# Optimization experiments

Measured on AMD Instinct MI355X. Metric: run time of the kernel, lower is better.

The kernel has to match this reference:

```python
import jax, jax.numpy as jnp
import numpy as np

N = 50000
E = 800000
IN_C = 512
HID = 256
NUM_CLASS = (10, 25, 16, 350)


def _glorot(key, shape):
    fan_in, fan_out = shape[0], shape[1]
    lim = float(np.sqrt(6.0 / (fan_in + fan_out)))
    return jax.random.uniform(key, shape, jnp.float32, -lim, lim)


def setup_inputs() -> dict:
    key = jax.random.key(0)
    ks = jax.random.split(key, 16)
    x = jax.random.normal(ks[0], (N, IN_C), jnp.float32)
    edge_index = jax.random.randint(ks[1], (2, E), 0, N, jnp.int32)
    inp = {"x": x, "edge_index": edge_index}
    # gc1
    inp["W1"] = _glorot(ks[2], (IN_C, HID)); inp["b1"] = jnp.zeros((HID,), jnp.float32)
    # four GCNConv heads
    names = ["type", "school", "time", "author"]
    for i, (nm, nc) in enumerate(zip(names, NUM_CLASS)):
        inp[f"Wg_{nm}"] = _glorot(ks[3 + i], (HID, nc))
        inp[f"bg_{nm}"] = jnp.zeros((nc,), jnp.float32)
        inp[f"Wc_{nm}"] = _glorot(ks[7 + i], (nc, nc))
        inp[f"bc_{nm}"] = jnp.zeros((nc,), jnp.float32)
    return inp


def gcn_conv(x, W, b, src, dst, n):
    # GCNConv: out = D^{-1/2} (A + I) D^{-1/2} (x W) + b, symmetric norm.
    xw = x @ W  # [N, out]
    ones = jnp.ones((src.shape[0],), xw.dtype)
    deg = jax.ops.segment_sum(ones, dst, num_segments=n) + 1.0  # +1 from self-loop
    dinv = jax.lax.rsqrt(deg)
    norm = dinv[src] * dinv[dst]  # [E]
    agg = jax.ops.segment_sum(xw[src] * norm[:, None], dst, num_segments=n)
    # self-loop contribution: norm_ii = dinv_i^2
    return agg + xw * (dinv * dinv)[:, None] + b


def reference(x, edge_index, W1, b1,
              Wg_type, bg_type, Wc_type, bc_type,
              Wg_school, bg_school, Wc_school, bc_school,
              Wg_time, bg_time, Wc_time, bc_time,
              Wg_author, bg_author, Wc_author, bc_author):
    src, dst = edge_index[0], edge_index[1]
    n = x.shape[0]
    h = jax.nn.relu(gcn_conv(x, W1, b1, src, dst, n))  # dropout is identity in eval

    def head(Wg, bg, Wc, bc):
        g = gcn_conv(h, Wg, bg, src, dst, n)
        return jax.nn.softmax(g @ Wc + bc, axis=-1)

    out_type = head(Wg_type, bg_type, Wc_type, bc_type)
    out_school = head(Wg_school, bg_school, Wc_school, bc_school)
    out_time = head(Wg_time, bg_time, Wc_time, bc_time)
    out_author = head(Wg_author, bg_author, Wc_author, bc_author)
    return (out_type, out_school, out_time, out_author)
```

## Files before the change

kernel.cpp:

```cpp
#include <hip/hip_runtime.h>
#include <hip/hip_bf16.h>
#include <cstdint>
#include <cstddef>
#include <math.h>

#define NN 50000
#define NE 800000
#define INC 512
#define HIDC 256
#define NBLK ((NN + 255) / 256)

typedef __attribute__((ext_vector_type(8))) short s8v;
typedef __attribute__((ext_vector_type(4))) float f4v;

__device__ __forceinline__ float b2f(unsigned short u) {
    return __uint_as_float(((unsigned)u) << 16);
}
__device__ __forceinline__ unsigned short f2b(float f) {
    __hip_bfloat16 h = __float2bfloat16(f);
    return *reinterpret_cast<unsigned short*>(&h);
}

__global__ void k_deg_count(const int* __restrict__ dst, int* __restrict__ cnt, int e) {
    int i = blockIdx.x * 256 + threadIdx.x;
    if (i < e) atomicAdd(&cnt[dst[i]], 1);
}
__global__ void k_scan1(const int* __restrict__ cnt, int* __restrict__ excl,
                        int* __restrict__ bsum, float* __restrict__ dinv, int n) {
    __shared__ int s[256];
    int i = blockIdx.x * 256 + threadIdx.x;
    int v = (i < n) ? cnt[i] : 0;
    if (i < n) dinv[i] = rsqrtf((float)v + 1.0f);
    s[threadIdx.x] = v;
    __syncthreads();
    for (int off = 1; off < 256; off <<= 1) {
        int t = (threadIdx.x >= off) ? s[threadIdx.x - off] : 0;
        __syncthreads();
        s[threadIdx.x] += t;
        __syncthreads();
    }
    if (i < n) excl[i] = s[threadIdx.x] - v;
    if (threadIdx.x == 255) bsum[blockIdx.x] = s[255];
}
__global__ void k_scan2(int* __restrict__ bsum, int* __restrict__ bsumx, int nb) {
    __shared__ int s[256];
    int t = threadIdx.x;
    int v = (t < nb) ? bsum[t] : 0;
    s[t] = v;
    __syncthreads();
    for (int off = 1; off < 256; off <<= 1) {
        int tt = (t >= off) ? s[t - off] : 0;
        __syncthreads();
        s[t] += tt;
        __syncthreads();
    }
    if (t < nb) bsumx[t] = s[t] - v;
}
__global__ void k_scan3(int* __restrict__ rowptr, const int* __restrict__ bsumx, int n, int e) {
    int i = blockIdx.x * 256 + threadIdx.x;
    if (i < n) rowptr[i] += bsumx[blockIdx.x];
    if (i == 0) rowptr[n] = e;
}
__global__ void k_fill(const int* __restrict__ src, const int* __restrict__ dst,
                       const int* __restrict__ rowptr, int* __restrict__ cursor,
                       int* __restrict__ col, int e) {
    int i = blockIdx.x * 256 + threadIdx.x;
    if (i >= e) return;
    int d = dst[i];
    int pos = rowptr[d] + atomicAdd(&cursor[d], 1);
    col[pos] = src[i];
}

__global__ void k_prep(const float* __restrict__ W1,
                       const float* __restrict__ Wg0, const float* __restrict__ Wc0,
                       const float* __restrict__ bg0, const float* __restrict__ bc0,
                       const float* __restrict__ Wg1, const float* __restrict__ Wc1,
                       const float* __restrict__ bg1, const float* __restrict__ bc1,
                       const float* __restrict__ Wg2, const float* __restrict__ Wc2,
                       const float* __restrict__ bg2, const float* __restrict__ bc2,
                       const float* __restrict__ Wg3, const float* __restrict__ Wc3,
                       const float* __restrict__ bg3, const float* __restrict__ bc3,
                       unsigned short* __restrict__ W1t, unsigned short* __restrict__ Wft,
                       float* __restrict__ bfv)
{
    int b = blockIdx.x, tid = threadIdx.x;
    if (b < 512) {
        int t = b * 256 + tid;
        int c = t >> 9, k = t & 511;
        W1t[t] = f2b(W1[(size_t)k * 256 + c]);
    } else if (b < 960) {
        int j = b - 512, k = tid;
        float s = 0.f;
        if (j < 350)                  { for (int i = 0; i < 350; ++i) s += Wg3[k * 350 + i] * Wc3[(size_t)i * 350 + j]; }
        else if (j >= 352 && j < 362) { int jj = j - 352; for (int i = 0; i < 10; ++i) s += Wg0[k * 10 + i] * Wc0[i * 10 + jj]; }
        else if (j >= 362 && j < 387) { int jj = j - 362; for (int i = 0; i < 25; ++i) s += Wg1[k * 25 + i] * Wc1[i * 25 + jj]; }
        else if (j >= 387 && j < 403) { int jj = j - 387; for (int i = 0; i < 16; ++i) s += Wg2[k * 16 + i] * Wc2[i * 16 + jj]; }
        Wft[j * 256 + k] = f2b(s);
    } else {
        int j = (b - 960) * 256 + tid;
        if (j >= 448) return;
        float s = 0.f;
        if (j < 350)                  { s = bc3[j]; for (int i = 0; i < 350; ++i) s += bg3[i] * Wc3[(size_t)i * 350 + j]; }
        else if (j >= 352 && j < 362) { int jj = j - 352; s = bc0[jj]; for (int i = 0; i < 10; ++i) s += bg0[i] * Wc0[i * 10 + jj]; }
        else if (j >= 362 && j < 387) { int jj = j - 362; s = bc1[jj]; for (int i = 0; i < 25; ++i) s += bg1[i] * Wc1[i * 25 + jj]; }
        else if (j >= 387 && j < 403) { int jj = j - 387; s = bc2[jj]; for (int i = 0; i < 16; ++i) s += bg2[i] * Wc2[i * 16 + jj]; }
        bfv[j] = s;
    }
}

__global__ __launch_bounds__(256) void gemm1_conv(
    const float* __restrict__ X, const unsigned short* __restrict__ Bt,
    unsigned short* __restrict__ C, int M)
{
    __shared__ s8v As[64 * 5];
    __shared__ s8v Bs[256 * 5];
    const int t = threadIdx.x;
    const int lane = t & 63, wv = t >> 6;
    const int row0 = blockIdx.x * 64;
    const int l15 = lane & 15, lq = lane >> 4;

    const int arow = t >> 2, ach = t & 3;
    int gr = row0 + arow; if (gr >= M) gr = M - 1;
    const float* asrc = X + (size_t)gr * 512 + ach * 8;

    f4v acc[16] = {};
    for (int k0 = 0; k0 < 512; k0 += 32) {
        {
            float4 a = *(const float4*)(asrc + k0);
            float4 b = *(const float4*)(asrc + k0 + 4);
            s8v o;
            o[0] = (short)f2b(a.x); o[1] = (short)f2b(a.y);
            o[2] = (short)f2b(a.z); o[3] = (short)f2b(a.w);
            o[4] = (short)f2b(b.x); o[5] = (short)f2b(b.y);
            o[6] = (short)f2b(b.z); o[7] = (short)f2b(b.w);
            As[arow * 5 + ach] = o;
        }
#pragma unroll
        for (int s = 0; s < 4; ++s) {
            int c = s * 256 + t;
            int colr = c >> 2, ch = c & 3;
            Bs[colr * 5 + ch] = *(const s8v*)(Bt + (size_t)colr * 512 + k0 + ch * 8);
        }
        __syncthreads();
        s8v af = As[(wv * 16 + l15) * 5 + lq];
#pragma unroll
        for (int cf = 0; cf < 16; ++cf) {
            s8v bfr = Bs[(cf * 16 + l15) * 5 + lq];
            acc[cf] = __builtin_amdgcn_mfma_f32_16x16x32_bf16(af, bfr, acc[cf], 0, 0, 0);
        }
        __syncthreads();
    }
#pragma unroll
    for (int cf = 0; cf < 16; ++cf)
#pragma unroll
        for (int r = 0; r < 4; ++r) {
            int row = row0 + wv * 16 + lq * 4 + r;
            if (row < M) C[(size_t)row * 256 + cf * 16 + l15] = f2b(acc[cf][r]);
        }
}

template <bool RELU, bool BIAS>
__global__ __launch_bounds__(256) void k_gather2(
    const unsigned short* __restrict__ feat, const int* __restrict__ rowptr,
    const int* __restrict__ col, const float* __restrict__ dinv,
    const float* __restrict__ bias, unsigned short* __restrict__ out, int n)
{
    int unit = (blockIdx.x * 256 + threadIdx.x) >> 5;
    int l32 = threadIdx.x & 31;
    if (unit >= n) return;
    float di = dinv[unit];
    int p0 = rowptr[unit], p1 = rowptr[unit + 1];
    int deg = p1 - p0;
    int myc = 0; float mydj = 0.f;
    if (l32 < deg) { myc = col[p0 + l32]; mydj = dinv[myc]; }
    float acc[8] = {};
    int dmin = deg < 32 ? deg : 32;
    int base = threadIdx.x & 32;
#pragma unroll 2
    for (int q = 0; q < dmin; ++q) {
        int j = __shfl(myc, base + q);
        float dj = __shfl(mydj, base + q);
        s8v v = *(const s8v*)(feat + (size_t)j * HIDC + l32 * 8);
#pragma unroll
        for (int c = 0; c < 8; ++c) acc[c] += dj * b2f((unsigned short)v[c]);
    }
    for (int p = p0 + 32; p < p1; ++p) {
        int j = col[p];
        float dj = dinv[j];
        s8v v = *(const s8v*)(feat + (size_t)j * HIDC + l32 * 8);
#pragma unroll
        for (int c = 0; c < 8; ++c) acc[c] += dj * b2f((unsigned short)v[c]);
    }
    s8v sv = *(const s8v*)(feat + (size_t)unit * HIDC + l32 * 8);
    float dd = di * di;
    s8v o;
#pragma unroll
    for (int c = 0; c < 8; ++c) {
        float r = di * acc[c] + dd * b2f((unsigned short)sv[c]);
        if (BIAS) r += bias[l32 * 8 + c];
        if (RELU) r = fmaxf(r, 0.f);
        o[c] = (short)f2b(r);
    }
    *(s8v*)(out + (size_t)unit * HIDC + l32 * 8) = o;
}

__global__ __launch_bounds__(256) void gemm2_heads(
    const unsigned short* __restrict__ A, const unsigned short* __restrict__ Bt,
    const float* __restrict__ bfv,
    float* __restrict__ o0, float* __restrict__ o1,
    float* __restrict__ o2, float* __restrict__ o3, int M)
{
    __shared__ s8v As[64 * 5];
    __shared__ s8v Bs[448 * 5];
    const int t = threadIdx.x;
    const int lane = t & 63, wv = t >> 6;
    const int row0 = blockIdx.x * 64;
    const int l15 = lane & 15, lq = lane >> 4;

    const int arow = t >> 2, ach = t & 3;
    int gr = row0 + arow; if (gr >= M) gr = M - 1;
    const unsigned short* asrc = A + (size_t)gr * 256 + ach * 8;

    f4v acc[28] = {};
    for (int k0 = 0; k0 < 256; k0 += 32) {
        As[arow * 5 + ach] = *(const s8v*)(asrc + k0);
#pragma unroll
        for (int s = 0; s < 7; ++s) {
            int c = s * 256 + t;
            int colr = c >> 2, ch = c & 3;
            Bs[colr * 5 + ch] = *(const s8v*)(Bt + (size_t)colr * 256 + k0 + ch * 8);
        }
        __syncthreads();
        s8v af = As[(wv * 16 + l15) * 5 + lq];
#pragma unroll
        for (int cf = 0; cf < 28; ++cf) {
            s8v bfr = Bs[(cf * 16 + l15) * 5 + lq];
            acc[cf] = __builtin_amdgcn_mfma_f32_16x16x32_bf16(af, bfr, acc[cf], 0, 0, 0);
        }
        __syncthreads();
    }
#pragma unroll
    for (int cf = 0; cf < 28; ++cf) {
        float b = bfv[cf * 16 + l15];
#pragma unroll
        for (int r = 0; r < 4; ++r) acc[cf][r] += b;
    }
#pragma unroll
    for (int r = 0; r < 4; ++r) {
        int row = row0 + wv * 16 + lq * 4 + r;
        float m0 = -1e30f, m1 = -1e30f, m2 = -1e30f, m3 = -1e30f;
#pragma unroll
        for (int cf = 0; cf < 28; ++cf) {
            int colc = cf * 16 + l15;
            float xv = acc[cf][r];
            if (colc < 350) m0 = fmaxf(m0, xv);
            else if (colc >= 352 && colc < 362) m1 = fmaxf(m1, xv);
            else if (colc >= 362 && colc < 387) m2 = fmaxf(m2, xv);
            else if (colc >= 387 && colc < 403) m3 = fmaxf(m3, xv);
        }
#pragma unroll
        for (int o = 8; o; o >>= 1) {
            m0 = fmaxf(m0, __shfl_xor(m0, o));
            m1 = fmaxf(m1, __shfl_xor(m1, o));
            m2 = fmaxf(m2, __shfl_xor(m2, o));
            m3 = fmaxf(m3, __shfl_xor(m3, o));
        }
        float s0 = 0.f, s1 = 0.f, s2 = 0.f, s3 = 0.f;
#pragma unroll
        for (int cf = 0; cf < 28; ++cf) {
            int colc = cf * 16 + l15;
            float xv = acc[cf][r];
            float e = 0.f;
            if (colc < 350)                     { e = __expf(xv - m0); s0 += e; }
            else if (colc >= 352 && colc < 362) { e = __expf(xv - m1); s1 += e; }
            else if (colc >= 362 && colc < 387) { e = __expf(xv - m2); s2 += e; }
            else if (colc >= 387 && colc < 403) { e = __expf(xv - m3); s3 += e; }
            acc[cf][r] = e;
        }
#pragma unroll
        for (int o = 8; o; o >>= 1) {
            s0 += __shfl_xor(s0, o); s1 += __shfl_xor(s1, o);
            s2 += __shfl_xor(s2, o); s3 += __shfl_xor(s3, o);
        }
        float i0 = 1.f / s0, i1 = 1.f / s1, i2 = 1.f / s2, i3 = 1.f / s3;
        if (row < M) {
#pragma unroll
            for (int cf = 0; cf < 28; ++cf) {
                int colc = cf * 16 + l15;
                float e = acc[cf][r];
                if (colc < 350)                     o3[(size_t)row * 350 + colc]       = e * i0;
                else if (colc >= 352 && colc < 362) o0[(size_t)row * 10 + colc - 352]  = e * i1;
                else if (colc >= 362 && colc < 387) o1[(size_t)row * 25 + colc - 362]  = e * i2;
                else if (colc >= 387 && colc < 403) o2[(size_t)row * 16 + colc - 387]  = e * i3;
            }
        }
    }
}

extern "C" void kernel_launch(void* const* d_in, const int* in_sizes, int n_in,
                              void* d_out, int out_size, void* d_ws, size_t ws_size,
                              hipStream_t stream)
{
    const float* x   = (const float*)d_in[0];
    const int*   ei  = (const int*)d_in[1];
    const float* W1  = (const float*)d_in[2];
    const float* b1  = (const float*)d_in[3];
    const float* Wg0 = (const float*)d_in[4];
    const float* bg0 = (const float*)d_in[5];
    const float* Wc0 = (const float*)d_in[6];
    const float* bc0 = (const float*)d_in[7];
    const float* Wg1 = (const float*)d_in[8];
    const float* bg1 = (const float*)d_in[9];
    const float* Wc1 = (const float*)d_in[10];
    const float* bc1 = (const float*)d_in[11];
    const float* Wg2 = (const float*)d_in[12];
    const float* bg2 = (const float*)d_in[13];
    const float* Wc2 = (const float*)d_in[14];
    const float* bc2 = (const float*)d_in[15];
    const float* Wg3 = (const float*)d_in[16];
    const float* bg3 = (const float*)d_in[17];
    const float* Wc3 = (const float*)d_in[18];
    const float* bc3 = (const float*)d_in[19];
    const int* srcI = ei;
    const int* dstI = ei + NE;

    char* ws = (char*)d_ws;
    size_t off = 0;
    auto alloc = [&](size_t bytes) { void* p = ws + off; off += (bytes + 255) & ~(size_t)255; return p; };
    float* dinv   = (float*)alloc(50176 * 4);
    int*   rowptr = (int*)  alloc(50432 * 4);
    int*   cnt    = (int*)  alloc(2 * 50176 * 4);
    int*   cursor = cnt + 50176;
    int*   bsum   = (int*)  alloc(1024);
    int*   bsumx  = (int*)  alloc(1024);
    int*   col    = (int*)  alloc((size_t)NE * 4);
    unsigned short* W1t = (unsigned short*)alloc(256 * 512 * 2);
    unsigned short* Wft = (unsigned short*)alloc(448 * 256 * 2);
    float* bfv   = (float*)alloc(448 * 4);
    unsigned short* xwb = (unsigned short*)alloc((size_t)NN * HIDC * 2);
    unsigned short* hb  = (unsigned short*)alloc((size_t)NN * HIDC * 2);
    unsigned short* ahb = xwb;

    float* out0 = (float*)d_out;
    float* out1 = out0 + (size_t)NN * 10;
    float* out2 = out1 + (size_t)NN * 25;
    float* out3 = out2 + (size_t)NN * 16;

    hipMemsetAsync(cnt, 0, 2 * 50176 * 4, stream);
    k_deg_count<<<(NE + 255) / 256, 256, 0, stream>>>(dstI, cnt, NE);
    k_scan1<<<NBLK, 256, 0, stream>>>(cnt, rowptr, bsum, dinv, NN);
    k_scan2<<<1, 256, 0, stream>>>(bsum, bsumx, NBLK);
    k_scan3<<<NBLK, 256, 0, stream>>>(rowptr, bsumx, NN, NE);
    k_fill<<<(NE + 255) / 256, 256, 0, stream>>>(srcI, dstI, rowptr, cursor, col, NE);

    k_prep<<<962, 256, 0, stream>>>(W1,
                                    Wg0, Wc0, bg0, bc0, Wg1, Wc1, bg1, bc1,
                                    Wg2, Wc2, bg2, bc2, Wg3, Wc3, bg3, bc3,
                                    W1t, Wft, bfv);

    gemm1_conv<<<(NN + 63) / 64, 256, 0, stream>>>(x, W1t, xwb, NN);
    k_gather2<true, true><<<(NN + 7) / 8, 256, 0, stream>>>(xwb, rowptr, col, dinv, b1, hb, NN);
    k_gather2<false, false><<<(NN + 7) / 8, 256, 0, stream>>>(hb, rowptr, col, dinv, nullptr, ahb, NN);
    gemm2_heads<<<(NN + 63) / 64, 256, 0, stream>>>(ahb, Wft, bfv, out0, out1, out2, out3, NN);
}
```

Before: 328.0 us.

## Swizzle LDS layouts, use direct global-to-LDS loads, retile both GEMMs across waves

Pre-swizzles the bf16 weight matrices (and the aggregated features feeding the head GEMM) into an XOR-swizzled chunk layout, so tiles can be copied straight into LDS with global_load_lds and read without bank conflicts. Both GEMMs now use a 2D wave tiling with 64-wide K steps: two row fragments share each B fragment, which halves LDS fragment reads and cuts the number of barriers. The head GEMM moves to 512 threads and reduces the softmax across waves through shared memory. Weight prep adds a transpose kernel so the 350x350 head-weight fold reads memory coalesced. The cost is more complex indexing, an extra small launch, and larger per-wave accumulator tiles.

```diff
diff --git a/kernel.cpp b/kernel.cpp
--- a/kernel.cpp
+++ b/kernel.cpp
@@ -12,6 +12,7 @@
 
 typedef __attribute__((ext_vector_type(8))) short s8v;
 typedef __attribute__((ext_vector_type(4))) float f4v;
+typedef unsigned int u32;
 
 __device__ __forceinline__ float b2f(unsigned short u) {
     return __uint_as_float(((unsigned)u) << 16);
@@ -19,6 +20,11 @@
 __device__ __forceinline__ unsigned short f2b(float f) {
     __hip_bfloat16 h = __float2bfloat16(f);
     return *reinterpret_cast<unsigned short*>(&h);
+}
+__device__ __forceinline__ void gload16(const void* g, void* l) {
+    __builtin_amdgcn_global_load_lds(
+        (const __attribute__((address_space(1))) u32*)g,
+        (__attribute__((address_space(3))) u32*)l, 16, 0, 0);
 }
 
 __global__ void k_deg_count(const int* __restrict__ dst, int* __restrict__ cnt, int e) {
@@ -71,6 +77,13 @@
     col[pos] = src[i];
 }
 
+__global__ void k_tr2(const float* __restrict__ Wg3, const float* __restrict__ Wc3,
+                      float* __restrict__ Wg3t, float* __restrict__ Wc3t) {
+    int t = blockIdx.x * 256 + threadIdx.x;
+    if (t < 256 * 350) { int k = t / 350, i = t - k * 350; Wg3t[i * 256 + k] = Wg3[t]; }
+    if (t < 350 * 350) { int i = t / 350, j = t - i * 350; Wc3t[j * 350 + i] = Wc3[t]; }
+}
+
 __global__ void k_prep(const float* __restrict__ W1,
                        const float* __restrict__ Wg0, const float* __restrict__ Wc0,
                        const float* __restrict__ bg0, const float* __restrict__ bc0,
@@ -80,22 +93,33 @@
                        const float* __restrict__ bg2, const float* __restrict__ bc2,
                        const float* __restrict__ Wg3, const float* __restrict__ Wc3,
                        const float* __restrict__ bg3, const float* __restrict__ bc3,
-                       unsigned short* __restrict__ W1t, unsigned short* __restrict__ Wft,
+                       const float* __restrict__ Wg3t, const float* __restrict__ Wc3t,
+                       unsigned short* __restrict__ W1t_sw, unsigned short* __restrict__ Wft_sw,
                        float* __restrict__ bfv)
 {
+    __shared__ float Wcj[352];
     int b = blockIdx.x, tid = threadIdx.x;
     if (b < 512) {
         int t = b * 256 + tid;
         int c = t >> 9, k = t & 511;
-        W1t[t] = f2b(W1[(size_t)k * 256 + c]);
+        int chs = ((k >> 3) & 7) ^ (c & 7);
+        W1t_sw[(size_t)(k >> 6) * 16384 + c * 64 + chs * 8 + (k & 7)] = f2b(W1[(size_t)k * 256 + c]);
     } else if (b < 960) {
         int j = b - 512, k = tid;
         float s = 0.f;
-        if (j < 350)                  { for (int i = 0; i < 350; ++i) s += Wg3[k * 350 + i] * Wc3[(size_t)i * 350 + j]; }
-        else if (j >= 352 && j < 362) { int jj = j - 352; for (int i = 0; i < 10; ++i) s += Wg0[k * 10 + i] * Wc0[i * 10 + jj]; }
-        else if (j >= 362 && j < 387) { int jj = j - 362; for (int i = 0; i < 25; ++i) s += Wg1[k * 25 + i] * Wc1[i * 25 + jj]; }
-        else if (j >= 387 && j < 403) { int jj = j - 387; for (int i = 0; i < 16; ++i) s += Wg2[k * 16 + i] * Wc2[i * 16 + jj]; }
-        Wft[j * 256 + k] = f2b(s);
+        if (j < 350) {
+            for (int i = tid; i < 350; i += 256) Wcj[i] = Wc3t[(size_t)j * 350 + i];
+            __syncthreads();
+            for (int i = 0; i < 350; ++i) s += Wg3t[i * 256 + k] * Wcj[i];
+        } else if (j >= 352 && j < 362) {
+            int jj = j - 352; for (int i = 0; i < 10; ++i) s += Wg0[k * 10 + i] * Wc0[i * 10 + jj];
+        } else if (j >= 362 && j < 387) {
+            int jj = j - 362; for (int i = 0; i < 25; ++i) s += Wg1[k * 25 + i] * Wc1[i * 25 + jj];
+        } else if (j >= 387 && j < 403) {
+            int jj = j - 387; for (int i = 0; i < 16; ++i) s += Wg2[k * 16 + i] * Wc2[i * 16 + jj];
+        }
+        int chs = ((k >> 3) & 7) ^ (j & 7);
+        Wft_sw[(size_t)(k >> 6) * 28672 + j * 64 + chs * 8 + (k & 7)] = f2b(s);
     } else {
         int j = (b - 960) * 256 + tid;
         if (j >= 448) return;
@@ -108,58 +132,69 @@
     }
 }
 
-__global__ __launch_bounds__(256) void gemm1_conv(
-    const float* __restrict__ X, const unsigned short* __restrict__ Bt,
+__global__ __launch_bounds__(256, 4) void gemm1_conv(
+    const float* __restrict__ X, const unsigned short* __restrict__ Bsw,
     unsigned short* __restrict__ C, int M)
 {
-    __shared__ s8v As[64 * 5];
-    __shared__ s8v Bs[256 * 5];
+    __shared__ s8v lds[512 + 2048];
     const int t = threadIdx.x;
     const int lane = t & 63, wv = t >> 6;
+    const int wvM = wv >> 1, wvN = wv & 1;
+    const int l15 = lane & 15, lq = lane >> 4;
     const int row0 = blockIdx.x * 64;
-    const int l15 = lane & 15, lq = lane >> 4;
-
-    const int arow = t >> 2, ach = t & 3;
+
+    const int arow = t >> 2;
     int gr = row0 + arow; if (gr >= M) gr = M - 1;
-    const float* asrc = X + (size_t)gr * 512 + ach * 8;
-
-    f4v acc[16] = {};
-    for (int k0 = 0; k0 < 512; k0 += 32) {
-        {
-            float4 a = *(const float4*)(asrc + k0);
-            float4 b = *(const float4*)(asrc + k0 + 4);
-            s8v o;
-            o[0] = (short)f2b(a.x); o[1] = (short)f2b(a.y);
-            o[2] = (short)f2b(a.z); o[3] = (short)f2b(a.w);
-            o[4] = (short)f2b(b.x); o[5] = (short)f2b(b.y);
-            o[6] = (short)f2b(b.z); o[7] = (short)f2b(b.w);
-            As[arow * 5 + ach] = o;
-        }
-#pragma unroll
-        for (int s = 0; s < 4; ++s) {
-            int c = s * 256 + t;
-            int colr = c >> 2, ch = c & 3;
-            Bs[colr * 5 + ch] = *(const s8v*)(Bt + (size_t)colr * 512 + k0 + ch * 8);
-        }
-        __syncthreads();
-        s8v af = As[(wv * 16 + l15) * 5 + lq];
-#pragma unroll
-        for (int cf = 0; cf < 16; ++cf) {
-            s8v bfr = Bs[(cf * 16 + l15) * 5 + lq];
-            acc[cf] = __builtin_amdgcn_mfma_f32_16x16x32_bf16(af, bfr, acc[cf], 0, 0, 0);
-        }
-        __syncthreads();
-    }
-#pragma unroll
-    for (int cf = 0; cf < 16; ++cf)
-#pragma unroll
-        for (int r = 0; r < 4; ++r) {
-            int row = row0 + wv * 16 + lq * 4 + r;
-            if (row < M) C[(size_t)row * 256 + cf * 16 + l15] = f2b(acc[cf][r]);
-        }
-}
-
-template <bool RELU, bool BIAS>
+    const float* asrc = X + (size_t)gr * INC + (t & 3) * 16;
+    const int ach0 = (t & 3) * 2;
+    s8v* aw0 = &lds[arow * 8 + (ach0 ^ (arow & 7))];
+    s8v* aw1 = &lds[arow * 8 + ((ach0 + 1) ^ (arow & 7))];
+
+    f4v acc[2][8] = {};
+    for (int kb = 0; kb < 8; ++kb) {
+        float4 f0 = *(const float4*)(asrc + kb * 64);
+        float4 f1 = *(const float4*)(asrc + kb * 64 + 4);
+        float4 f2 = *(const float4*)(asrc + kb * 64 + 8);
+        float4 f3 = *(const float4*)(asrc + kb * 64 + 12);
+        s8v o0, o1;
+        o0[0]=(short)f2b(f0.x); o0[1]=(short)f2b(f0.y); o0[2]=(short)f2b(f0.z); o0[3]=(short)f2b(f0.w);
+        o0[4]=(short)f2b(f1.x); o0[5]=(short)f2b(f1.y); o0[6]=(short)f2b(f1.z); o0[7]=(short)f2b(f1.w);
+        o1[0]=(short)f2b(f2.x); o1[1]=(short)f2b(f2.y); o1[2]=(short)f2b(f2.z); o1[3]=(short)f2b(f2.w);
+        o1[4]=(short)f2b(f3.x); o1[5]=(short)f2b(f3.y); o1[6]=(short)f2b(f3.z); o1[7]=(short)f2b(f3.w);
+        *aw0 = o0; *aw1 = o1;
+#pragma unroll
+        for (int sB = 0; sB < 8; ++sB) {
+            int ci = (wv * 8 + sB) * 64 + lane;
+            gload16(Bsw + ((size_t)kb * 2048 + ci) * 8, (void*)&lds[512 + (wv * 8 + sB) * 64]);
+        }
+        __syncthreads();
+#pragma unroll
+        for (int kk = 0; kk < 2; ++kk) {
+            const int chr = (kk * 4 + lq) ^ (l15 & 7);
+            s8v a0 = lds[(wvM * 32 + l15) * 8 + chr];
+            s8v a1 = lds[(wvM * 32 + 16 + l15) * 8 + chr];
+#pragma unroll
+            for (int cf = 0; cf < 8; ++cf) {
+                s8v bf = lds[512 + (wvN * 128 + cf * 16 + l15) * 8 + chr];
+                acc[0][cf] = __builtin_amdgcn_mfma_f32_16x16x32_bf16(a0, bf, acc[0][cf], 0, 0, 0);
+                acc[1][cf] = __builtin_amdgcn_mfma_f32_16x16x32_bf16(a1, bf, acc[1][cf], 0, 0, 0);
+            }
+        }
+        __syncthreads();
+    }
+#pragma unroll
+    for (int rf = 0; rf < 2; ++rf)
+#pragma unroll
+    for (int r = 0; r < 4; ++r) {
+        int row = row0 + wvM * 32 + rf * 16 + lq * 4 + r;
+        if (row >= M) continue;
+#pragma unroll
+        for (int cf = 0; cf < 8; ++cf)
+            C[(size_t)row * HIDC + wvN * 128 + cf * 16 + l15] = f2b(acc[rf][cf][r]);
+    }
+}
+
+template <bool RELU, bool BIAS, bool SWZ>
 __global__ __launch_bounds__(256) void k_gather2(
     const unsigned short* __restrict__ feat, const int* __restrict__ rowptr,
     const int* __restrict__ col, const float* __restrict__ dinv,
@@ -201,98 +236,155 @@
         if (RELU) r = fmaxf(r, 0.f);
         o[c] = (short)f2b(r);
     }
-    *(s8v*)(out + (size_t)unit * HIDC + l32 * 8) = o;
-}
-
-__global__ __launch_bounds__(256) void gemm2_heads(
-    const unsigned short* __restrict__ A, const unsigned short* __restrict__ Bt,
+    int outch = SWZ ? ((l32 & 24) | ((l32 & 7) ^ (unit & 7))) : l32;
+    *(s8v*)(out + (size_t)unit * HIDC + outch * 8) = o;
+}
+
+__global__ __launch_bounds__(512, 4) void gemm2_heads(
+    const unsigned short* __restrict__ Asw, const unsigned short* __restrict__ Bsw,
     const float* __restrict__ bfv,
     float* __restrict__ o0, float* __restrict__ o1,
     float* __restrict__ o2, float* __restrict__ o3, int M)
 {
-    __shared__ s8v As[64 * 5];
-    __shared__ s8v Bs[448 * 5];
+    __shared__ s8v lds[512 + 3584];
     const int t = threadIdx.x;
     const int lane = t & 63, wv = t >> 6;
+    const int wvM = wv >> 2, wvN = wv & 3;
+    const int l15 = lane & 15, lq = lane >> 4;
     const int row0 = blockIdx.x * 64;
-    const int l15 = lane & 15, lq = lane >> 4;
-
-    const int arow = t >> 2, ach = t & 3;
-    int gr = row0 + arow; if (gr >= M) gr = M - 1;
-    const unsigned short* asrc = A + (size_t)gr * 256 + ach * 8;
-
-    f4v acc[28] = {};
-    for (int k0 = 0; k0 < 256; k0 += 32) {
-        As[arow * 5 + ach] = *(const s8v*)(asrc + k0);
-#pragma unroll
-        for (int s = 0; s < 7; ++s) {
-            int c = s * 256 + t;
-            int colr = c >> 2, ch = c & 3;
-            Bs[colr * 5 + ch] = *(const s8v*)(Bt + (size_t)colr * 256 + k0 + ch * 8);
-        }
-        __syncthreads();
-        s8v af = As[(wv * 16 + l15) * 5 + lq];
-#pragma unroll
-        for (int cf = 0; cf < 28; ++cf) {
-            s8v bfr = Bs[(cf * 16 + l15) * 5 + lq];
-            acc[cf] = __builtin_amdgcn_mfma_f32_16x16x32_bf16(af, bfr, acc[cf], 0, 0, 0);
-        }
-        __syncthreads();
-    }
-#pragma unroll
-    for (int cf = 0; cf < 28; ++cf) {
-        float b = bfv[cf * 16 + l15];
-#pragma unroll
-        for (int r = 0; r < 4; ++r) acc[cf][r] += b;
-    }
+
+    f4v acc[2][7] = {};
+    for (int kb = 0; kb < 4; ++kb) {
+        {
+            int ci = wv * 64 + lane;
+            int arow = ci >> 3, ch = ci & 7;
+            int grow = row0 + arow; if (grow >= M) grow = M - 1;
+            gload16(Asw + (size_t)grow * HIDC + (kb * 8 + ch) * 8, (void*)&lds[wv * 64]);
+        }
+#pragma unroll
+        for (int sB = 0; sB < 7; ++sB) {
+            int ci = (wv * 7 + sB) * 64 + lane;
+            gload16(Bsw + ((size_t)kb * 3584 + ci) * 8, (void*)&lds[512 + (wv * 7 + sB) * 64]);
+        }
+        __syncthreads();
+#pragma unroll
+        for (int kk = 0; kk < 2; ++kk) {
+            const int chr = (kk * 4 + lq) ^ (l15 & 7);
+            s8v a0 = lds[(wvM * 32 + l15) * 8 + chr];
+            s8v a1 = lds[(wvM * 32 + 16 + l15) * 8 + chr];
+#pragma unroll
+            for (int cf = 0; cf < 7; ++cf) {
+                s8v bf = lds[512 + (wvN * 112 + cf * 16 + l15) * 8 + chr];
+                acc[0][cf] = __builtin_amdgcn_mfma_f32_16x16x32_bf16(a0, bf, acc[0][cf], 0, 0, 0);
+                acc[1][cf] = __builtin_amdgcn_mfma_f32_16x16x32_bf16(a1, bf, acc[1][cf], 0, 0, 0);
+            }
+        }
+        __syncthreads();
+    }
+    float* smx = (float*)lds;
+#pragma unroll
+    for (int cf = 0; cf < 7; ++cf) {
+        float bb = bfv[wvN * 112 + cf * 16 + l15];
+#pragma unroll
+        for (int rf = 0; rf < 2; ++rf)
+#pragma unroll
+        for (int r = 0; r < 4; ++r) acc[rf][cf][r] += bb;
+    }
+#pragma unroll
+    for (int rf = 0; rf < 2; ++rf)
 #pragma unroll
     for (int r = 0; r < 4; ++r) {
-        int row = row0 + wv * 16 + lq * 4 + r;
-        float m0 = -1e30f, m1 = -1e30f, m2 = -1e30f, m3 = -1e30f;
-#pragma unroll
-        for (int cf = 0; cf < 28; ++cf) {
-            int colc = cf * 16 + l15;
-            float xv = acc[cf][r];
-            if (colc < 350) m0 = fmaxf(m0, xv);
-            else if (colc >= 352 && colc < 362) m1 = fmaxf(m1, xv);
-            else if (colc >= 362 && colc < 387) m2 = fmaxf(m2, xv);
-            else if (colc >= 387 && colc < 403) m3 = fmaxf(m3, xv);
+        float ma = -1e30f, m1 = -1e30f, m2 = -1e30f, m3 = -1e30f;
+#pragma unroll
+        for (int cf = 0; cf < 7; ++cf) {
+            int colc = wvN * 112 + cf * 16 + l15;
+            float v = acc[rf][cf][r];
+            if (colc < 350) ma = fmaxf(ma, v);
+            else if (colc >= 352 && colc < 362) m1 = fmaxf(m1, v);
+            else if (colc >= 362 && colc < 387) m2 = fmaxf(m2, v);
+            else if (colc >= 387 && colc < 403) m3 = fmaxf(m3, v);
         }
 #pragma unroll
         for (int o = 8; o; o >>= 1) {
-            m0 = fmaxf(m0, __shfl_xor(m0, o));
+            ma = fmaxf(ma, __shfl_xor(ma, o));
             m1 = fmaxf(m1, __shfl_xor(m1, o));
             m2 = fmaxf(m2, __shfl_xor(m2, o));
             m3 = fmaxf(m3, __shfl_xor(m3, o));
         }
-        float s0 = 0.f, s1 = 0.f, s2 = 0.f, s3 = 0.f;
-#pragma unroll
-        for (int cf = 0; cf < 28; ++cf) {
-            int colc = cf * 16 + l15;
-            float xv = acc[cf][r];
+        int rowl = wvM * 32 + rf * 16 + lq * 4 + r;
+        if (l15 == 0) {
+            smx[rowl * 4 + wvN] = ma;
+            if (wvN == 3) {
+                smx[512 + rowl * 3 + 0] = m1;
+                smx[512 + rowl * 3 + 1] = m2;
+                smx[512 + rowl * 3 + 2] = m3;
+            }
+        }
+    }
+    __syncthreads();
+#pragma unroll
+    for (int rf = 0; rf < 2; ++rf)
+#pragma unroll
+    for (int r = 0; r < 4; ++r) {
+        int rowl = wvM * 32 + rf * 16 + lq * 4 + r;
+        float am = fmaxf(fmaxf(smx[rowl * 4 + 0], smx[rowl * 4 + 1]),
+                         fmaxf(smx[rowl * 4 + 2], smx[rowl * 4 + 3]));
+        float m1 = 0.f, m2 = 0.f, m3 = 0.f;
+        if (wvN == 3) {
+            m1 = smx[512 + rowl * 3 + 0];
+            m2 = smx[512 + rowl * 3 + 1];
+            m3 = smx[512 + rowl * 3 + 2];
+        }
+        float sa = 0.f, s1 = 0.f, s2 = 0.f, s3 = 0.f;
+#pragma unroll
+        for (int cf = 0; cf < 7; ++cf) {
+            int colc = wvN * 112 + cf * 16 + l15;
+            float v = acc[rf][cf][r];
             float e = 0.f;
-            if (colc < 350)                     { e = __expf(xv - m0); s0 += e; }
-            else if (colc >= 352 && colc < 362) { e = __expf(xv - m1); s1 += e; }
-            else if (colc >= 362 && colc < 387) { e = __expf(xv - m2); s2 += e; }
-            else if (colc >= 387 && colc < 403) { e = __expf(xv - m3); s3 += e; }
-            acc[cf][r] = e;
+            if (colc < 350)                     { e = __expf(v - am); sa += e; }
+            else if (colc >= 352 && colc < 362) { e = __expf(v - m1); s1 += e; }
+            else if (colc >= 362 && colc < 387) { e = __expf(v - m2); s2 += e; }
+            else if (colc >= 387 && colc < 403) { e = __expf(v - m3); s3 += e; }
+            acc[rf][cf][r] = e;
         }
 #pragma unroll
         for (int o = 8; o; o >>= 1) {
-            s0 += __shfl_xor(s0, o); s1 += __shfl_xor(s1, o);
+            sa += __shfl_xor(sa, o); s1 += __shfl_xor(s1, o);
             s2 += __shfl_xor(s2, o); s3 += __shfl_xor(s3, o);
         }
-        float i0 = 1.f / s0, i1 = 1.f / s1, i2 = 1.f / s2, i3 = 1.f / s3;
-        if (row < M) {
-#pragma unroll
-            for (int cf = 0; cf < 28; ++cf) {
-                int colc = cf * 16 + l15;
-                float e = acc[cf][r];
-                if (colc < 350)                     o3[(size_t)row * 350 + colc]       = e * i0;
-                else if (colc >= 352 && colc < 362) o0[(size_t)row * 10 + colc - 352]  = e * i1;
-                else if (colc >= 362 && colc < 387) o1[(size_t)row * 25 + colc - 362]  = e * i2;
-                else if (colc >= 387 && colc < 403) o2[(size_t)row * 16 + colc - 387]  = e * i3;
+        if (l15 == 0) {
+            smx[256 + rowl * 4 + wvN] = sa;
+            if (wvN == 3) {
+                smx[704 + rowl * 3 + 0] = s1;
+                smx[704 + rowl * 3 + 1] = s2;
+                smx[704 + rowl * 3 + 2] = s3;
             }
+        }
+    }
+    __syncthreads();
+#pragma unroll
+    for (int rf = 0; rf < 2; ++rf)
+#pragma unroll
+    for (int r = 0; r < 4; ++r) {
+        int rowl = wvM * 32 + rf * 16 + lq * 4 + r;
+        int row = row0 + rowl;
+        if (row >= M) continue;
+        float ia = 1.f / (smx[256 + rowl * 4 + 0] + smx[256 + rowl * 4 + 1] +
+                          smx[256 + rowl * 4 + 2] + smx[256 + rowl * 4 + 3]);
+        float i1 = 0.f, i2 = 0.f, i3 = 0.f;
+        if (wvN == 3) {
+            i1 = 1.f / smx[704 + rowl * 3 + 0];
+            i2 = 1.f / smx[704 + rowl * 3 + 1];
+            i3 = 1.f / smx[704 + rowl * 3 + 2];
+        }
+#pragma unroll
+        for (int cf = 0; cf < 7; ++cf) {
+            int colc = wvN * 112 + cf * 16 + l15;
+            float e = acc[rf][cf][r];
+            if (colc < 350)                     o3[(size_t)row * 350 + colc]        = e * ia;
+            else if (colc >= 352 && colc < 362) o0[(size_t)row * 10 + (colc - 352)] = e * i1;
+            else if (colc >= 362 && colc < 387) o1[(size_t)row * 25 + (colc - 362)] = e * i2;
+            else if (colc >= 387 && colc < 403) o2[(size_t)row * 16 + (colc - 387)] = e * i3;
         }
     }
 }
@@ -334,9 +426,11 @@
     int*   bsum   = (int*)  alloc(1024);
     int*   bsumx  = (int*)  alloc(1024);
     int*   col    = (int*)  alloc((size_t)NE * 4);
-    unsigned short* W1t = (unsigned short*)alloc(256 * 512 * 2);
-    unsigned short* Wft = (unsigned short*)alloc(448 * 256 * 2);
+    unsigned short* W1t_sw = (unsigned short*)alloc(256 * 512 * 2);
+    unsigned short* Wft_sw = (unsigned short*)alloc(448 * 256 * 2);
     float* bfv   = (float*)alloc(448 * 4);
+    float* Wg3t  = (float*)alloc(350 * 256 * 4);
+    float* Wc3t  = (float*)alloc(350 * 350 * 4);
     unsigned short* xwb = (unsigned short*)alloc((size_t)NN * HIDC * 2);
     unsigned short* hb  = (unsigned short*)alloc((size_t)NN * HIDC * 2);
     unsigned short* ahb = xwb;
@@ -353,13 +447,14 @@
     k_scan3<<<NBLK, 256, 0, stream>>>(rowptr, bsumx, NN, NE);
     k_fill<<<(NE + 255) / 256, 256, 0, stream>>>(srcI, dstI, rowptr, cursor, col, NE);
 
+    k_tr2<<<(350 * 350 + 255) / 256, 256, 0, stream>>>(Wg3, Wc3, Wg3t, Wc3t);
     k_prep<<<962, 256, 0, stream>>>(W1,
                                     Wg0, Wc0, bg0, bc0, Wg1, Wc1, bg1, bc1,
                                     Wg2, Wc2, bg2, bc2, Wg3, Wc3, bg3, bc3,
-                                    W1t, Wft, bfv);
-
-    gemm1_conv<<<(NN + 63) / 64, 256, 0, stream>>>(x, W1t, xwb, NN);
-    k_gather2<true, true><<<(NN + 7) / 8, 256, 0, stream>>>(xwb, rowptr, col, dinv, b1, hb, NN);
-    k_gather2<false, false><<<(NN + 7) / 8, 256, 0, stream>>>(hb, rowptr, col, dinv, nullptr, ahb, NN);
-    gemm2_heads<<<(NN + 63) / 64, 256, 0, stream>>>(ahb, Wft, bfv, out0, out1, out2, out3, NN);
-}
+                                    Wg3t, Wc3t, W1t_sw, Wft_sw, bfv);
+
+    gemm1_conv<<<(NN + 63) / 64, 256, 0, stream>>>(x, W1t_sw, xwb, NN);
+    k_gather2<true, true, false><<<(NN + 7) / 8, 256, 0, stream>>>(xwb, rowptr, col, dinv, b1, hb, NN);
+    k_gather2<false, false, true><<<(NN + 7) / 8, 256, 0, stream>>>(hb, rowptr, col, dinv, nullptr, ahb, NN);
+    gemm2_heads<<<(NN + 63) / 64, 512, 0, stream>>>(ahb, Wft_sw, bfv, out0, out1, out2, out3, NN);
+}
```

New measurement: 341.7 us. 1.04x slower.
